# Performance work log

Hardware: AMD Instinct MI355X
Metric: run time of the kernel (lower is better)

The kernel has to match this reference:

```python
import jax, jax.numpy as jnp
import numpy as np
from jax import lax

B, S, L = 128, 256, 10
WORD, CHAR = 50000, 100
TAGS, START, END = 32, 30, 31
WDIM, CDIM, FILT, H = 100, 30, 30, 100
LSTM_IN = WDIM + FILT  # 130
NEG = -10000.0


def setup_inputs() -> dict:
    key = jax.random.key(0)
    ks = jax.random.split(key, 24)
    sc = 0.1
    word_emb = (jax.random.normal(ks[0], (WORD, WDIM), jnp.float32) * sc).at[0].set(0.0)  # padding_idx=0
    char_emb = (jax.random.normal(ks[1], (CHAR, CDIM), jnp.float32) * sc).at[0].set(0.0)
    conv_w = jax.random.normal(ks[2], (FILT, 1, 3, CDIM), jnp.float32) * sc  # OIHW, kernel (3, char_dim)
    conv_b = jax.random.normal(ks[3], (FILT,), jnp.float32) * sc
    wih_f = jax.random.normal(ks[4], (4 * H, LSTM_IN), jnp.float32) * sc
    whh_f = jax.random.normal(ks[5], (4 * H, H), jnp.float32) * sc
    bih_f = jax.random.normal(ks[6], (4 * H,), jnp.float32) * sc
    bhh_f = jax.random.normal(ks[7], (4 * H,), jnp.float32) * sc
    wih_b = jax.random.normal(ks[8], (4 * H, LSTM_IN), jnp.float32) * sc
    whh_b = jax.random.normal(ks[9], (4 * H, H), jnp.float32) * sc
    bih_b = jax.random.normal(ks[10], (4 * H,), jnp.float32) * sc
    bhh_b = jax.random.normal(ks[11], (4 * H,), jnp.float32) * sc
    proj_w = jax.random.normal(ks[12], (TAGS, 2 * H), jnp.float32) * sc
    proj_b = jax.random.normal(ks[13], (TAGS,), jnp.float32) * sc
    trans = jax.random.normal(ks[14], (TAGS, TAGS), jnp.float32)
    trans = trans.at[:, START].set(NEG).at[END, :].set(NEG)  # CRF.reset_parm
    word_x = jax.random.randint(ks[15], (B, S), 1, WORD, jnp.int32)
    char_x = jax.random.randint(ks[16], (B, S, L), 1, CHAR, jnp.int32)
    y = jax.random.randint(ks[17], (B, S), 0, 30, jnp.int32)  # gold tags exclude start/end
    mask = jnp.ones((B, S), jnp.int32)
    return dict(word_emb=word_emb, char_emb=char_emb, conv_w=conv_w, conv_b=conv_b,
                wih_f=wih_f, whh_f=whh_f, bih_f=bih_f, bhh_f=bhh_f,
                wih_b=wih_b, whh_b=whh_b, bih_b=bih_b, bhh_b=bhh_b,
                proj_w=proj_w, proj_b=proj_b, trans=trans,
                word_x=word_x, char_x=char_x, y=y, mask=mask)


def _lstm_dir(x, wih, whh, bih, bhh, reverse):
    # x: [B, S, D] -> hidden states [B, S, H]; PyTorch gate order i, f, g, o
    b = bih + bhh
    xs = jnp.swapaxes(x, 0, 1)  # [S, B, D]
    if reverse:
        xs = xs[::-1]
    Bv = x.shape[0]
    Hd = whh.shape[1]
    init = (jnp.zeros((Bv, Hd), x.dtype), jnp.zeros((Bv, Hd), x.dtype))
    def step(carry, xt):
        h, c = carry
        g = xt @ wih.T + h @ whh.T + b  # [B, 4H]
        i, f, gg, o = jnp.split(g, 4, axis=-1)
        c = jax.nn.sigmoid(f) * c + jax.nn.sigmoid(i) * jnp.tanh(gg)
        h = jax.nn.sigmoid(o) * jnp.tanh(c)
        return (h, c), h
    _, hs = lax.scan(step, init, xs)
    if reverse:
        hs = hs[::-1]
    return jnp.swapaxes(hs, 0, 1)


def _forward(word_emb, char_emb, conv_w, conv_b, wih_f, whh_f, bih_f, bhh_f,
             wih_b, whh_b, bih_b, bhh_b, proj_w, proj_b, trans,
             word_x, char_x, y, mask):
    # --- CharCNN (dropout = identity in eval) ---
    ce = char_emb[char_x].reshape(B * S, 1, L, CDIM)  # [B*S, 1, L, CDIM]
    fm = lax.conv_general_dilated(ce, conv_w, (1, 1), ((2, 2), (0, 0)),
                                  dimension_numbers=('NCHW', 'OIHW', 'NCHW'))
    fm = fm + conv_b[None, :, None, None]  # [B*S, FILT, L+2, 1]
    char_feat = fm.max(axis=(2, 3)).reshape(B, S, FILT)
    # --- BiLSTM + projection ---
    x = jnp.concatenate([word_emb[word_x], char_feat], axis=-1)  # [B, S, 130]
    h_f = _lstm_dir(x, wih_f, whh_f, bih_f, bhh_f, False)
    h_b = _lstm_dir(x, wih_b, whh_b, bih_b, bhh_b, True)
    emission = jnp.concatenate([h_f, h_b], axis=-1) @ proj_w.T + proj_b  # [B, S, TAGS]
    maskf = mask.astype(emission.dtype)
    # --- CRF gold-path score (vectorized form of compute_y_score) ---
    y_pad = jnp.concatenate([jnp.full((B, 1), START, y.dtype), y], axis=1)  # [B, S+1]
    prev, cur = y_pad[:, :-1], y_pad[:, 1:]
    p = jnp.take_along_axis(emission, cur[..., None].astype(jnp.int32), axis=-1)[..., 0]
    t = trans[prev, cur]
    score_y = ((p + t) * maskf).sum(axis=1) + trans[y[:, -1], END]  # original uses last label unmasked
    # --- CRF partition function (logsumexp scan over time) ---
    la0 = jnp.full((B, TAGS), NEG, emission.dtype).at[:, START].set(0.0)
    def step(la, em_m):
        em, m = em_m  # em: [B, TAGS], m: [B]
        la2 = jax.nn.logsumexp(la[:, :, None] + trans[None, :, :] + em[:, None, :], axis=1)
        m = m[:, None]
        return la2 * m + la * (1.0 - m), None
    la, _ = lax.scan(step, la0, (jnp.swapaxes(emission, 0, 1), maskf.T))
    la = la + trans[:, END][None, :]
    total = jax.nn.logsumexp(la, axis=1, keepdims=True)  # [B, 1]
    # faithful to original: [B] - [B,1] broadcasts to [B,B], then mean
    return -jnp.mean(score_y - total)


def reference(word_emb, char_emb, conv_w, conv_b, wih_f, whh_f, bih_f, bhh_f,
              wih_b, whh_b, bih_b, bhh_b, proj_w, proj_b, trans,
              word_x, char_x, y, mask):
    return _forward(word_emb, char_emb, conv_w, conv_b, wih_f, whh_f, bih_f, bhh_f,
                    wih_b, whh_b, bih_b, bhh_b, proj_w, proj_b, trans,
                    word_x, char_x, y, mask)
```

## Files before the change

### kernel.cpp

```cpp
#include <hip/hip_runtime.h>
#include <hip/hip_fp16.h>
#include <cstdint>
#include <cstddef>

#define BB 128
#define SS 256
#define LL 10
#define NTAGS 32
#define TAG_START 30
#define TAG_END 31
#define WDIM 100
#define CDIM 30
#define NFILT 30
#define HDIM 100
#define KIN 130
#define KPAD 160
#define GDIM 400
#define NROWS 832
#define NEGV -10000.0f
#define CTOK 8

#define NB_CONV (BB * SS / CTOK)
#define NB_WORD (BB * SS * KPAD / 256)
#define NB_WCVT (NROWS * KPAD / 256)
#define NB_PRE  (NB_CONV + NB_WORD + NB_WCVT)

typedef _Float16 h2 __attribute__((ext_vector_type(2)));
typedef _Float16 f16x8 __attribute__((ext_vector_type(8)));
typedef float f32x4 __attribute__((ext_vector_type(4)));

#if __has_builtin(__builtin_amdgcn_fdot2)
#define HAVE_FDOT2 1
#else
#define HAVE_FDOT2 0
#endif

__device__ __forceinline__ float sigm(float x) { return 1.0f / (1.0f + __expf(-x)); }
__device__ __forceinline__ float tanh_fast(float x) { return 2.0f / (1.0f + __expf(-2.0f * x)) - 1.0f; }

__device__ __forceinline__ void barrier_lds_only() {
  asm volatile("s_waitcnt lgkmcnt(0)" ::: "memory");
  __builtin_amdgcn_s_barrier();
  asm volatile("" ::: "memory");
}

__global__ __launch_bounds__(256) void k_pre(
    const float* __restrict__ wemb, const int* __restrict__ wx,
    const float* __restrict__ cemb, const float* __restrict__ convw,
    const float* __restrict__ convb, const int* __restrict__ cx,
    const float* __restrict__ wihF, const float* __restrict__ wihB,
    _Float16* __restrict__ x16, _Float16* __restrict__ w16,
    float* __restrict__ out) {
  int blk = blockIdx.x;
  int tid = threadIdx.x;
  if (blk == 0 && tid == 0) out[0] = 0.f;

  if (blk < NB_CONV) {
    int tok8 = tid >> 5;
    int f = tid & 31;
    int token0 = blk * CTOK;
    __shared__ float e[CTOK][LL * CDIM];
    __shared__ float cw[NFILT * 3 * CDIM];
    __shared__ float cb[NFILT];
    __shared__ int ci[CTOK][LL];
    if (tid < CTOK * LL) {
      int t = tid / LL, l = tid - t * LL;
      ci[t][l] = cx[(token0 + t) * LL + l];
    }
    for (int i = tid; i < NFILT * 3 * CDIM; i += 256) cw[i] = convw[i];
    if (tid < NFILT) cb[tid] = convb[tid];
    __syncthreads();
    for (int i = tid; i < CTOK * LL * CDIM; i += 256) {
      int t = i / (LL * CDIM);
      int r = i - t * (LL * CDIM);
      int l = r / CDIM, c = r - l * CDIM;
      e[t][l * CDIM + c] = cemb[ci[t][l] * CDIM + c];
    }
    __syncthreads();
    if (f < NFILT) {
      float d0[LL], d1[LL], d2[LL];
#pragma unroll
      for (int l = 0; l < LL; l++) { d0[l] = 0.f; d1[l] = 0.f; d2[l] = 0.f; }
      const float* et = &e[tok8][0];
      for (int c = 0; c < CDIM; c++) {
        float w0 = cw[(f * 3 + 0) * CDIM + c];
        float w1 = cw[(f * 3 + 1) * CDIM + c];
        float w2 = cw[(f * 3 + 2) * CDIM + c];
#pragma unroll
        for (int l = 0; l < LL; l++) {
          float ev = et[l * CDIM + c];
          d0[l] += ev * w0; d1[l] += ev * w1; d2[l] += ev * w2;
        }
      }
      float bias = cb[f];
      float m = -3.0e38f;
#pragma unroll
      for (int h = 0; h < LL + 2; h++) {
        float acc = bias;
        int j0 = h - 2, j1 = h - 1, j2 = h;
        if (j0 >= 0 && j0 < LL) acc += d0[j0];
        if (j1 >= 0 && j1 < LL) acc += d1[j1];
        if (j2 >= 0 && j2 < LL) acc += d2[j2];
        m = fmaxf(m, acc);
      }
      x16[(size_t)(token0 + tok8) * KPAD + WDIM + f] = (_Float16)m;
    }
  } else if (blk < NB_CONV + NB_WORD) {
    int idx = (blk - NB_CONV) * 256 + tid;
    int token = idx / KPAD;
    int d = idx - token * KPAD;
    if (d < WDIM) {
      x16[idx] = (_Float16)wemb[(size_t)wx[token] * WDIM + d];
    } else if (d >= KIN) {
      x16[idx] = (_Float16)0.f;
    }
  } else {
    int idx = (blk - NB_CONV - NB_WORD) * 256 + tid;
    int n = idx / KPAD;
    int k = idx - n * KPAD;
    float v = 0.f;
    if (k < KIN && n < 2 * GDIM) {
      v = (n < GDIM) ? wihF[(size_t)n * KIN + k] : wihB[(size_t)(n - GDIM) * KIN + k];
    }
    w16[idx] = (_Float16)v;
  }
}

__global__ __launch_bounds__(256) void k_pregemm(
    const _Float16* __restrict__ x16, const _Float16* __restrict__ w16,
    const float* __restrict__ bihF, const float* __restrict__ bhhF,
    const float* __restrict__ bihB, const float* __restrict__ bhhB,
    _Float16* __restrict__ preF, _Float16* __restrict__ preB) {
  __shared__ __align__(16) _Float16 Asl[64 * 40];
  __shared__ __align__(16) _Float16 Bsl[64 * 40];
  int m0 = blockIdx.x * 64;
  int n0 = blockIdx.y * 64;
  int tid = threadIdx.x;
  int lane = tid & 63, w = tid >> 6;
  int quad = lane >> 4, l15 = lane & 15;

  f32x4 acc[4];
#pragma unroll
  for (int i = 0; i < 4; i++) acc[i] = (f32x4){0.f, 0.f, 0.f, 0.f};

  int r = tid >> 2;
  int kk = (tid & 3) * 8;
  const _Float16* xs = x16 + (size_t)(m0 + r) * KPAD + kk;
  const _Float16* wsrc = w16 + (size_t)(n0 + r) * KPAD + kk;

  for (int kc = 0; kc < 5; kc++) {
    if (kc) __syncthreads();
    *(f16x8*)&Asl[r * 40 + kk] = *(const f16x8*)(xs + kc * 32);
    *(f16x8*)&Bsl[r * 40 + kk] = *(const f16x8*)(wsrc + kc * 32);
    __syncthreads();

    f16x8 bfrag = *(const f16x8*)&Bsl[(w * 16 + l15) * 40 + quad * 8];
#pragma unroll
    for (int mt = 0; mt < 4; mt++) {
      f16x8 afrag = *(const f16x8*)&Asl[(mt * 16 + l15) * 40 + quad * 8];
      acc[mt] = __builtin_amdgcn_mfma_f32_16x16x32_f16(afrag, bfrag, acc[mt], 0, 0, 0);
    }
  }

  int ng = n0 + w * 16 + l15;
  if (ng < 2 * GDIM) {
    int dir = ng >= GDIM;
    int jb = dir ? ng - GDIM : ng;
    _Float16* dst = dir ? preB : preF;
    float bias = (dir ? bihB : bihF)[jb] + (dir ? bhhB : bhhF)[jb];
#pragma unroll
    for (int mt = 0; mt < 4; mt++) {
#pragma unroll
      for (int i = 0; i < 4; i++) {
        int m = m0 + mt * 16 + quad * 4 + i;
        dst[(size_t)m * GDIM + jb] = (_Float16)(acc[mt][i] + bias);
      }
    }
  }
}

#define CH 32
#define NCH (SS / CH)
__global__ __launch_bounds__(256, 1) void k_lstm(
    const _Float16* __restrict__ preF, const _Float16* __restrict__ preB,
    const float* __restrict__ whhF, const float* __restrict__ whhB,
    _Float16* __restrict__ hbuf) {
  int blk = blockIdx.x;
  int dir = blk >> 7;
  int b = blk & 127;
  const _Float16* pre = dir ? preB : preF;
  const float* whh = dir ? whhB : whhF;
  int tid = threadIdx.x;
  int j = tid >> 1;
  int kh = tid & 1;
  bool act = (j < HDIM);
  int jc = act ? j : 0;

  __half2 wp[4][25];
#pragma unroll
  for (int g = 0; g < 4; g++) {
    const float* wr = whh + (size_t)(g * HDIM + jc) * HDIM + kh * 50;
#pragma unroll
    for (int q = 0; q < 25; q++) {
      wp[g][q] = __floats2half2_rn(wr[2 * q], wr[2 * q + 1]);
    }
  }

  __shared__ __align__(16) _Float16 preS[14336];
  __shared__ __align__(16) _Float16 hsh[2][2][64];
  if (tid < 128) ((int*)hsh)[tid] = 0;
  float c = 0.f;

#define GSRC(ck) ((const uint4*)(pre + ((size_t)b * SS + (dir ? (SS - CH - (ck) * CH) : ((ck) * CH))) * GDIM))

  uint4 r0, r1, r2, r3, r4, r5, r6;
  {
    const uint4* s0 = GSRC(0);
    r0 = s0[0 * 256 + tid]; r1 = s0[1 * 256 + tid]; r2 = s0[2 * 256 + tid];
    r3 = s0[3 * 256 + tid]; r4 = s0[4 * 256 + tid]; r5 = s0[5 * 256 + tid];
    r6 = s0[6 * 256 + tid];
  }

  _Float16* hptr = hbuf + ((size_t)b * SS + (dir ? (SS - 1) : 0)) * (2 * HDIM) + dir * HDIM + jc;
  const intptr_t hstep = dir ? -(intptr_t)(2 * HDIM) : (intptr_t)(2 * HDIM);

  int cur = 0;
  for (int ck = 0; ck < NCH; ck++) {
    asm volatile("s_waitcnt vmcnt(0)" ::: "memory");
    *(uint4*)&preS[(0 * 256 + tid) * 8] = r0;
    *(uint4*)&preS[(1 * 256 + tid) * 8] = r1;
    *(uint4*)&preS[(2 * 256 + tid) * 8] = r2;
    *(uint4*)&preS[(3 * 256 + tid) * 8] = r3;
    *(uint4*)&preS[(4 * 256 + tid) * 8] = r4;
    *(uint4*)&preS[(5 * 256 + tid) * 8] = r5;
    *(uint4*)&preS[(6 * 256 + tid) * 8] = r6;
    if (ck + 1 < NCH) {
      const uint4* snx = GSRC(ck + 1);
      r0 = snx[0 * 256 + tid]; r1 = snx[1 * 256 + tid]; r2 = snx[2 * 256 + tid];
      r3 = snx[3 * 256 + tid]; r4 = snx[4 * 256 + tid]; r5 = snx[5 * 256 + tid];
      r6 = snx[6 * 256 + tid];
    }
    barrier_lds_only();

    int preOff = (dir ? (CH - 1) * GDIM : 0) + kh * 200 + jc;
    const int pdelta = dir ? -GDIM : GDIM;

    for (int s2 = 0; s2 < CH; s2++) {
      float paF = (float)preS[preOff];
      float pbF = (float)preS[preOff + 100];

      const _Float16* hseg = &hsh[cur][kh][0];
      uint4 hv0 = *(const uint4*)(hseg);
      uint4 hv1 = *(const uint4*)(hseg + 8);
      uint4 hv2 = *(const uint4*)(hseg + 16);
      uint4 hv3 = *(const uint4*)(hseg + 24);
      uint4 hv4 = *(const uint4*)(hseg + 32);
      uint4 hv5 = *(const uint4*)(hseg + 40);
      uint32_t hv6 = *(const uint32_t*)(hseg + 48);
      __half2 hp[25];
      hp[0]  = __builtin_bit_cast(__half2, hv0.x);
      hp[1]  = __builtin_bit_cast(__half2, hv0.y);
      hp[2]  = __builtin_bit_cast(__half2, hv0.z);
      hp[3]  = __builtin_bit_cast(__half2, hv0.w);
      hp[4]  = __builtin_bit_cast(__half2, hv1.x);
      hp[5]  = __builtin_bit_cast(__half2, hv1.y);
      hp[6]  = __builtin_bit_cast(__half2, hv1.z);
      hp[7]  = __builtin_bit_cast(__half2, hv1.w);
      hp[8]  = __builtin_bit_cast(__half2, hv2.x);
      hp[9]  = __builtin_bit_cast(__half2, hv2.y);
      hp[10] = __builtin_bit_cast(__half2, hv2.z);
      hp[11] = __builtin_bit_cast(__half2, hv2.w);
      hp[12] = __builtin_bit_cast(__half2, hv3.x);
      hp[13] = __builtin_bit_cast(__half2, hv3.y);
      hp[14] = __builtin_bit_cast(__half2, hv3.z);
      hp[15] = __builtin_bit_cast(__half2, hv3.w);
      hp[16] = __builtin_bit_cast(__half2, hv4.x);
      hp[17] = __builtin_bit_cast(__half2, hv4.y);
      hp[18] = __builtin_bit_cast(__half2, hv4.z);
      hp[19] = __builtin_bit_cast(__half2, hv4.w);
      hp[20] = __builtin_bit_cast(__half2, hv5.x);
      hp[21] = __builtin_bit_cast(__half2, hv5.y);
      hp[22] = __builtin_bit_cast(__half2, hv5.z);
      hp[23] = __builtin_bit_cast(__half2, hv5.w);
      hp[24] = __builtin_bit_cast(__half2, hv6);

      float racc[4];
#if HAVE_FDOT2
#pragma unroll
      for (int g = 0; g < 4; g++) {
        float a0 = 0.f, a1 = 0.f;
#pragma unroll
        for (int q = 0; q < 25; q += 2)
          a0 = __builtin_amdgcn_fdot2(__builtin_bit_cast(h2, wp[g][q]),
                                      __builtin_bit_cast(h2, hp[q]), a0, false);
#pragma unroll
        for (int q = 1; q < 25; q += 2)
          a1 = __builtin_amdgcn_fdot2(__builtin_bit_cast(h2, wp[g][q]),
                                      __builtin_bit_cast(h2, hp[q]), a1, false);
        racc[g] = a0 + a1;
      }
#else
      __half2 z = __floats2half2_rn(0.f, 0.f);
#pragma unroll
      for (int g = 0; g < 4; g++) {
        __half2 a0 = z, a1 = z;
#pragma unroll
        for (int q = 0; q < 25; q += 2) a0 = __hfma2(wp[g][q], hp[q], a0);
#pragma unroll
        for (int q = 1; q < 25; q += 2) a1 = __hfma2(wp[g][q], hp[q], a1);
        racc[g] = (__low2float(a0) + __high2float(a0)) +
                  (__low2float(a1) + __high2float(a1));
      }
#endif

      if (kh == 0) { racc[0] += paF; racc[1] += pbF; }
      else         { racc[2] += paF; racc[3] += pbF; }
#pragma unroll
      for (int g = 0; g < 4; g++) racc[g] += __shfl_xor(racc[g], 1);

      float ig = sigm(racc[0]), fg = sigm(racc[1]);
      float g2 = tanh_fast(racc[2]), og = sigm(racc[3]);
      c = fg * c + ig * g2;
      float h = og * tanh_fast(c);

      if (act && kh == 0) {
        int seg = (j >= 50) ? 1 : 0;
        hsh[cur ^ 1][seg][j - seg * 50] = (_Float16)h;
        *hptr = (_Float16)h;
      }

      barrier_lds_only();
      cur ^= 1;
      preOff += pdelta;
      hptr += hstep;
    }
  }
#undef GSRC
}

__global__ __launch_bounds__(256) void k_proj(const _Float16* __restrict__ hbuf,
                                              const float* __restrict__ pw,
                                              const float* __restrict__ pb,
                                              float* __restrict__ em) {
  __shared__ __align__(16) float pws[NTAGS * 204];
  __shared__ float pbs[NTAGS];
  int tid = threadIdx.x;
  for (int i = tid; i < NTAGS * 2 * HDIM; i += 256) {
    int tag = i / (2 * HDIM);
    int k = i - tag * (2 * HDIM);
    pws[tag * 204 + k] = pw[i];
  }
  if (tid < NTAGS) pbs[tid] = pb[tid];
  __syncthreads();

  int idx = blockIdx.x * blockDim.x + tid;
  if (idx >= BB * SS * NTAGS) return;
  int token = idx >> 5, tag = idx & 31;
  const uint4* h4 = (const uint4*)(hbuf + (size_t)token * 2 * HDIM);
  const float4* w4 = (const float4*)&pws[tag * 204];
  float acc = pbs[tag];
#pragma unroll
  for (int k = 0; k < 25; k++) {
    uint4 hv = h4[k];
    h2 a = __builtin_bit_cast(h2, hv.x);
    h2 bq = __builtin_bit_cast(h2, hv.y);
    h2 cq = __builtin_bit_cast(h2, hv.z);
    h2 d = __builtin_bit_cast(h2, hv.w);
    float4 w0 = w4[k * 2], w1 = w4[k * 2 + 1];
    acc += (float)a.x * w0.x + (float)a.y * w0.y + (float)bq.x * w0.z + (float)bq.y * w0.w
         + (float)cq.x * w1.x + (float)cq.y * w1.y + (float)d.x * w1.z + (float)d.y * w1.w;
  }
  em[idx] = acc;
}

__global__ __launch_bounds__(64) void k_crf(const float* __restrict__ em,
                                            const float* __restrict__ trans,
                                            const int* __restrict__ mask,
                                            const int* __restrict__ y,
                                            float* __restrict__ out) {
  int b = blockIdx.x;
  int lane = threadIdx.x;
  int j = lane & 31;
  int h = lane >> 5;

  __shared__ __align__(16) float emS[SS * NTAGS];
  __shared__ __align__(16) int mkS[SS];
  {
    const uint4* src = (const uint4*)(em + (size_t)b * SS * NTAGS);
#pragma unroll
    for (int p = 0; p < 32; p++) {
      uint4 t = src[p * 64 + lane];
      *(uint4*)&emS[(p * 64 + lane) * 4] = t;
    }
    uint4 mv = ((const uint4*)(mask + (size_t)b * SS))[lane];
    *(uint4*)&mkS[lane * 4] = mv;
  }
  barrier_lds_only();

  float sacc = 0.f;
  for (int s = lane; s < SS; s += 64) {
    int curt = y[b * SS + s];
    int prevt = (s == 0) ? TAG_START : y[b * SS + s - 1];
    float mk = (float)mkS[s];
    sacc += (emS[s * NTAGS + curt] + trans[prevt * NTAGS + curt]) * mk;
  }
#pragma unroll
  for (int off = 32; off > 0; off >>= 1) sacc += __shfl_down(sacc, off);
  float scoreYv = __shfl(sacc, 0) + trans[y[b * SS + SS - 1] * NTAGS + TAG_END];

  float tcol[16];
#pragma unroll
  for (int i = 0; i < 16; i++) tcol[i] = trans[(h * 16 + i) * NTAGS + j];

  float la = (j == TAG_START) ? 0.f : NEGV;

  for (int s = 0; s < SS; s++) {
    float e0 = emS[s * NTAGS + j];
    float mkv = (float)mkS[s];

    float v[16];
#pragma unroll
    for (int i = 0; i < 16; i++) v[i] = __shfl(la, h * 16 + i) + tcol[i];

    float ma = v[0], mb2 = v[1];
#pragma unroll
    for (int i = 2; i < 16; i += 2) { ma = fmaxf(ma, v[i]); mb2 = fmaxf(mb2, v[i + 1]); }
    float mh = fmaxf(ma, mb2);
    float m = fmaxf(mh, __shfl_xor(mh, 32));

    float sa = 0.f, sb = 0.f;
#pragma unroll
    for (int i = 0; i < 16; i += 2) { sa += __expf(v[i] - m); sb += __expf(v[i + 1] - m); }
    float sh = sa + sb;
    float sum = sh + __shfl_xor(sh, 32);

    float la2 = m + __logf(sum) + e0;
    la = la2 * mkv + la * (1.f - mkv);
  }
  la += trans[j * NTAGS + TAG_END];

  float mm = la;
#pragma unroll
  for (int off = 16; off > 0; off >>= 1) mm = fmaxf(mm, __shfl_xor(mm, off));
  float ss = __expf(la - mm);
#pragma unroll
  for (int off = 16; off > 0; off >>= 1) ss += __shfl_xor(ss, off);
  float total = mm + __logf(ss);
  if (lane == 0) atomicAdd(out, (total - scoreYv) * (1.0f / BB));
}

extern "C" void kernel_launch(void* const* d_in, const int* in_sizes, int n_in,
                              void* d_out, int out_size, void* d_ws, size_t ws_size,
                              hipStream_t stream) {
  const float* word_emb = (const float*)d_in[0];
  const float* char_emb = (const float*)d_in[1];
  const float* conv_w   = (const float*)d_in[2];
  const float* conv_b   = (const float*)d_in[3];
  const float* wih_f    = (const float*)d_in[4];
  const float* whh_f    = (const float*)d_in[5];
  const float* bih_f    = (const float*)d_in[6];
  const float* bhh_f    = (const float*)d_in[7];
  const float* wih_b    = (const float*)d_in[8];
  const float* whh_b    = (const float*)d_in[9];
  const float* bih_b    = (const float*)d_in[10];
  const float* bhh_b    = (const float*)d_in[11];
  const float* proj_w   = (const float*)d_in[12];
  const float* proj_b   = (const float*)d_in[13];
  const float* trans    = (const float*)d_in[14];
  const int* word_x     = (const int*)d_in[15];
  const int* char_x     = (const int*)d_in[16];
  const int* y          = (const int*)d_in[17];
  const int* mask       = (const int*)d_in[18];
  float* out = (float*)d_out;

  _Float16* x16   = (_Float16*)d_ws;
  _Float16* w16   = x16 + (size_t)BB * SS * KPAD;
  _Float16* preF  = w16 + (size_t)NROWS * KPAD;
  _Float16* preB  = preF + (size_t)BB * SS * GDIM;
  _Float16* hbuf  = preB + (size_t)BB * SS * GDIM;
  float* em       = (float*)(hbuf + (size_t)BB * SS * 2 * HDIM);

  k_pre<<<NB_PRE, 256, 0, stream>>>(word_emb, word_x, char_emb, conv_w, conv_b,
                                    char_x, wih_f, wih_b, x16, w16, out);
  k_pregemm<<<dim3(BB * SS / 64, 13), 256, 0, stream>>>(x16, w16, bih_f, bhh_f,
                                                        bih_b, bhh_b, preF, preB);
  k_lstm<<<256, 256, 0, stream>>>(preF, preB, whh_f, whh_b, hbuf);
  k_proj<<<(BB * SS * NTAGS + 255) / 256, 256, 0, stream>>>(hbuf, proj_w, proj_b, em);
  k_crf<<<BB, 64, 0, stream>>>(em, trans, mask, y, out);
}
```

Measured before the change: 495.2 us.

## Split LSTM recurrent dot product across four lanes per hidden unit

The recurrent LSTM kernel now uses 448 threads per block, with four lanes per hidden unit, each covering 26 of the 100 hidden inputs instead of two lanes covering 50. This shortens the serial dot-product chain per time step, trading it for an extra shuffle-reduction round and padded zero work. The preactivation chunk staging is remapped to the larger thread count, with a partial fourth load.

```diff
diff --git a/kernel.cpp b/kernel.cpp
--- a/kernel.cpp
+++ b/kernel.cpp
@@ -181,7 +181,8 @@
 
 #define CH 32
 #define NCH (SS / CH)
-__global__ __launch_bounds__(256, 1) void k_lstm(
+#define LSTM_NT 448
+__global__ __launch_bounds__(LSTM_NT, 1) void k_lstm(
     const _Float16* __restrict__ preF, const _Float16* __restrict__ preB,
     const float* __restrict__ whhF, const float* __restrict__ whhB,
     _Float16* __restrict__ hbuf) {
@@ -191,34 +192,39 @@
   const _Float16* pre = dir ? preB : preF;
   const float* whh = dir ? whhB : whhF;
   int tid = threadIdx.x;
-  int j = tid >> 1;
-  int kh = tid & 1;
-  bool act = (j < HDIM);
-  int jc = act ? j : 0;
-
-  __half2 wp[4][25];
+  int j = tid >> 2;
+  int kq = tid & 3;
+  bool jv = (j < HDIM);
+  int jc = jv ? j : 0;
+
+  __half2 wf[4][16];
 #pragma unroll
   for (int g = 0; g < 4; g++) {
-    const float* wr = whh + (size_t)(g * HDIM + jc) * HDIM + kh * 50;
-#pragma unroll
-    for (int q = 0; q < 25; q++) {
-      wp[g][q] = __floats2half2_rn(wr[2 * q], wr[2 * q + 1]);
-    }
-  }
-
-  __shared__ __align__(16) _Float16 preS[14336];
-  __shared__ __align__(16) _Float16 hsh[2][2][64];
-  if (tid < 128) ((int*)hsh)[tid] = 0;
+    const float* wr = whh + (size_t)(g * HDIM + jc) * HDIM;
+#pragma unroll
+    for (int e = 0; e < 16; e++) {
+      int k = kq * 26 + 2 * e;
+      float w0 = (jv && e < 13 && k < HDIM) ? wr[k] : 0.f;
+      float w1 = (jv && e < 13 && k + 1 < HDIM) ? wr[k + 1] : 0.f;
+      wf[g][e] = __floats2half2_rn(w0, w1);
+    }
+  }
+
+  __shared__ __align__(16) _Float16 preS[CH * GDIM];
+  __shared__ __align__(16) _Float16 hsh[2][4][32];
+  for (int i = tid; i < 2 * 4 * 32 / 2; i += LSTM_NT) ((int*)hsh)[i] = 0;
   float c = 0.f;
 
 #define GSRC(ck) ((const uint4*)(pre + ((size_t)b * SS + (dir ? (SS - CH - (ck) * CH) : ((ck) * CH))) * GDIM))
 
-  uint4 r0, r1, r2, r3, r4, r5, r6;
+  uint4 r0, r1, r2, r3;
+  r3 = (uint4){0, 0, 0, 0};
   {
     const uint4* s0 = GSRC(0);
-    r0 = s0[0 * 256 + tid]; r1 = s0[1 * 256 + tid]; r2 = s0[2 * 256 + tid];
-    r3 = s0[3 * 256 + tid]; r4 = s0[4 * 256 + tid]; r5 = s0[5 * 256 + tid];
-    r6 = s0[6 * 256 + tid];
+    r0 = s0[0 * LSTM_NT + tid];
+    r1 = s0[1 * LSTM_NT + tid];
+    r2 = s0[2 * LSTM_NT + tid];
+    if (tid < 1600 - 3 * LSTM_NT) r3 = s0[3 * LSTM_NT + tid];
   }
 
   _Float16* hptr = hbuf + ((size_t)b * SS + (dir ? (SS - 1) : 0)) * (2 * HDIM) + dir * HDIM + jc;
@@ -227,62 +233,44 @@
   int cur = 0;
   for (int ck = 0; ck < NCH; ck++) {
     asm volatile("s_waitcnt vmcnt(0)" ::: "memory");
-    *(uint4*)&preS[(0 * 256 + tid) * 8] = r0;
-    *(uint4*)&preS[(1 * 256 + tid) * 8] = r1;
-    *(uint4*)&preS[(2 * 256 + tid) * 8] = r2;
-    *(uint4*)&preS[(3 * 256 + tid) * 8] = r3;
-    *(uint4*)&preS[(4 * 256 + tid) * 8] = r4;
-    *(uint4*)&preS[(5 * 256 + tid) * 8] = r5;
-    *(uint4*)&preS[(6 * 256 + tid) * 8] = r6;
+    *(uint4*)&preS[(0 * LSTM_NT + tid) * 8] = r0;
+    *(uint4*)&preS[(1 * LSTM_NT + tid) * 8] = r1;
+    *(uint4*)&preS[(2 * LSTM_NT + tid) * 8] = r2;
+    if (tid < 1600 - 3 * LSTM_NT) *(uint4*)&preS[(3 * LSTM_NT + tid) * 8] = r3;
     if (ck + 1 < NCH) {
       const uint4* snx = GSRC(ck + 1);
-      r0 = snx[0 * 256 + tid]; r1 = snx[1 * 256 + tid]; r2 = snx[2 * 256 + tid];
-      r3 = snx[3 * 256 + tid]; r4 = snx[4 * 256 + tid]; r5 = snx[5 * 256 + tid];
-      r6 = snx[6 * 256 + tid];
+      r0 = snx[0 * LSTM_NT + tid];
+      r1 = snx[1 * LSTM_NT + tid];
+      r2 = snx[2 * LSTM_NT + tid];
+      if (tid < 1600 - 3 * LSTM_NT) r3 = snx[3 * LSTM_NT + tid];
     }
     barrier_lds_only();
 
-    int preOff = (dir ? (CH - 1) * GDIM : 0) + kh * 200 + jc;
+    int preOff = (dir ? (CH - 1) * GDIM : 0) + kq * 100 + jc;
     const int pdelta = dir ? -GDIM : GDIM;
 
     for (int s2 = 0; s2 < CH; s2++) {
-      float paF = (float)preS[preOff];
-      float pbF = (float)preS[preOff + 100];
-
-      const _Float16* hseg = &hsh[cur][kh][0];
-      uint4 hv0 = *(const uint4*)(hseg);
-      uint4 hv1 = *(const uint4*)(hseg + 8);
-      uint4 hv2 = *(const uint4*)(hseg + 16);
-      uint4 hv3 = *(const uint4*)(hseg + 24);
-      uint4 hv4 = *(const uint4*)(hseg + 32);
-      uint4 hv5 = *(const uint4*)(hseg + 40);
-      uint32_t hv6 = *(const uint32_t*)(hseg + 48);
-      __half2 hp[25];
-      hp[0]  = __builtin_bit_cast(__half2, hv0.x);
-      hp[1]  = __builtin_bit_cast(__half2, hv0.y);
-      hp[2]  = __builtin_bit_cast(__half2, hv0.z);
-      hp[3]  = __builtin_bit_cast(__half2, hv0.w);
-      hp[4]  = __builtin_bit_cast(__half2, hv1.x);
-      hp[5]  = __builtin_bit_cast(__half2, hv1.y);
-      hp[6]  = __builtin_bit_cast(__half2, hv1.z);
-      hp[7]  = __builtin_bit_cast(__half2, hv1.w);
-      hp[8]  = __builtin_bit_cast(__half2, hv2.x);
-      hp[9]  = __builtin_bit_cast(__half2, hv2.y);
-      hp[10] = __builtin_bit_cast(__half2, hv2.z);
-      hp[11] = __builtin_bit_cast(__half2, hv2.w);
-      hp[12] = __builtin_bit_cast(__half2, hv3.x);
-      hp[13] = __builtin_bit_cast(__half2, hv3.y);
-      hp[14] = __builtin_bit_cast(__half2, hv3.z);
-      hp[15] = __builtin_bit_cast(__half2, hv3.w);
-      hp[16] = __builtin_bit_cast(__half2, hv4.x);
-      hp[17] = __builtin_bit_cast(__half2, hv4.y);
-      hp[18] = __builtin_bit_cast(__half2, hv4.z);
-      hp[19] = __builtin_bit_cast(__half2, hv4.w);
-      hp[20] = __builtin_bit_cast(__half2, hv5.x);
-      hp[21] = __builtin_bit_cast(__half2, hv5.y);
-      hp[22] = __builtin_bit_cast(__half2, hv5.z);
-      hp[23] = __builtin_bit_cast(__half2, hv5.w);
-      hp[24] = __builtin_bit_cast(__half2, hv6);
+      float p = (float)preS[preOff];
+
+      const uint4* hw = (const uint4*)&hsh[cur][kq][0];
+      uint4 h0 = hw[0], h1 = hw[1], h2v = hw[2], h3 = hw[3];
+      __half2 hp[16];
+      hp[0]  = __builtin_bit_cast(__half2, h0.x);
+      hp[1]  = __builtin_bit_cast(__half2, h0.y);
+      hp[2]  = __builtin_bit_cast(__half2, h0.z);
+      hp[3]  = __builtin_bit_cast(__half2, h0.w);
+      hp[4]  = __builtin_bit_cast(__half2, h1.x);
+      hp[5]  = __builtin_bit_cast(__half2, h1.y);
+      hp[6]  = __builtin_bit_cast(__half2, h1.z);
+      hp[7]  = __builtin_bit_cast(__half2, h1.w);
+      hp[8]  = __builtin_bit_cast(__half2, h2v.x);
+      hp[9]  = __builtin_bit_cast(__half2, h2v.y);
+      hp[10] = __builtin_bit_cast(__half2, h2v.z);
+      hp[11] = __builtin_bit_cast(__half2, h2v.w);
+      hp[12] = __builtin_bit_cast(__half2, h3.x);
+      hp[13] = __builtin_bit_cast(__half2, h3.y);
+      hp[14] = __builtin_bit_cast(__half2, h3.z);
+      hp[15] = __builtin_bit_cast(__half2, h3.w);
 
       float racc[4];
 #if HAVE_FDOT2
@@ -290,12 +278,12 @@
       for (int g = 0; g < 4; g++) {
         float a0 = 0.f, a1 = 0.f;
 #pragma unroll
-        for (int q = 0; q < 25; q += 2)
-          a0 = __builtin_amdgcn_fdot2(__builtin_bit_cast(h2, wp[g][q]),
+        for (int q = 0; q < 16; q += 2)
+          a0 = __builtin_amdgcn_fdot2(__builtin_bit_cast(h2, wf[g][q]),
                                       __builtin_bit_cast(h2, hp[q]), a0, false);
 #pragma unroll
-        for (int q = 1; q < 25; q += 2)
-          a1 = __builtin_amdgcn_fdot2(__builtin_bit_cast(h2, wp[g][q]),
+        for (int q = 1; q < 16; q += 2)
+          a1 = __builtin_amdgcn_fdot2(__builtin_bit_cast(h2, wf[g][q]),
                                       __builtin_bit_cast(h2, hp[q]), a1, false);
         racc[g] = a0 + a1;
       }
@@ -305,27 +293,30 @@
       for (int g = 0; g < 4; g++) {
         __half2 a0 = z, a1 = z;
 #pragma unroll
-        for (int q = 0; q < 25; q += 2) a0 = __hfma2(wp[g][q], hp[q], a0);
-#pragma unroll
-        for (int q = 1; q < 25; q += 2) a1 = __hfma2(wp[g][q], hp[q], a1);
+        for (int q = 0; q < 16; q += 2) a0 = __hfma2(wf[g][q], hp[q], a0);
+#pragma unroll
+        for (int q = 1; q < 16; q += 2) a1 = __hfma2(wf[g][q], hp[q], a1);
         racc[g] = (__low2float(a0) + __high2float(a0)) +
                   (__low2float(a1) + __high2float(a1));
       }
 #endif
 
-      if (kh == 0) { racc[0] += paF; racc[1] += pbF; }
-      else         { racc[2] += paF; racc[3] += pbF; }
-#pragma unroll
-      for (int g = 0; g < 4; g++) racc[g] += __shfl_xor(racc[g], 1);
+#pragma unroll
+      for (int g = 0; g < 4; g++) racc[g] += (kq == g) ? p : 0.f;
+#pragma unroll
+      for (int g = 0; g < 4; g++) {
+        racc[g] += __shfl_xor(racc[g], 1);
+        racc[g] += __shfl_xor(racc[g], 2);
+      }
 
       float ig = sigm(racc[0]), fg = sigm(racc[1]);
       float g2 = tanh_fast(racc[2]), og = sigm(racc[3]);
       c = fg * c + ig * g2;
       float h = og * tanh_fast(c);
 
-      if (act && kh == 0) {
-        int seg = (j >= 50) ? 1 : 0;
-        hsh[cur ^ 1][seg][j - seg * 50] = (_Float16)h;
+      if (jv && kq == 0) {
+        int wdw = j / 26;
+        hsh[cur ^ 1][wdw][j - wdw * 26] = (_Float16)h;
         *hptr = (_Float16)h;
       }
 
@@ -484,7 +475,7 @@
                                     char_x, wih_f, wih_b, x16, w16, out);
   k_pregemm<<<dim3(BB * SS / 64, 13), 256, 0, stream>>>(x16, w16, bih_f, bhh_f,
                                                         bih_b, bhh_b, preF, preB);
-  k_lstm<<<256, 256, 0, stream>>>(preF, preB, whh_f, whh_b, hbuf);
+  k_lstm<<<256, LSTM_NT, 0, stream>>>(preF, preB, whh_f, whh_b, hbuf);
   k_proj<<<(BB * SS * NTAGS + 255) / 256, 256, 0, stream>>>(hbuf, proj_w, proj_b, em);
   k_crf<<<BB, 64, 0, stream>>>(em, trans, mask, y, out);
 }
```

After: 599.3 us. 1.21x slower.
